# Optimization experiments

Measured on AMD Instinct MI355X. Metric: run time of the kernel, lower is better.

Reference implementation:

```python
import jax, jax.numpy as jnp
import numpy as np

NUM_LEVELS = 2
RADIUS = 3


def setup_inputs() -> dict:
    key = jax.random.key(0)
    k1, k2, k3 = jax.random.split(key, 3)
    x = jax.random.normal(k1, (4, 320, 9, 32, 32), dtype=jnp.float32)
    w_fc0 = jax.random.normal(k2, (160, 320), dtype=jnp.float32) * 0.05
    w_fc1 = jax.random.normal(k3, (160, 320), dtype=jnp.float32) * 0.05
    return {"x": x, "w_fc0": w_fc0, "w_fc1": w_fc1}


def _bilinear_zeros(img, xs, ys):
    # img: (M, H, W); xs, ys: (M, K) pixel coords.
    # Matches F.grid_sample(mode='bilinear', padding_mode='zeros', align_corners=True):
    # align_corners normalization round-trips to the raw pixel coords, and
    # out-of-bounds corners contribute zero.
    M, H, W = img.shape
    x0f = jnp.floor(xs)
    y0f = jnp.floor(ys)
    wx = xs - x0f
    wy = ys - y0f
    x0 = x0f.astype(jnp.int32)
    y0 = y0f.astype(jnp.int32)
    x1 = x0 + 1
    y1 = y0 + 1
    n = jnp.arange(M)[:, None]

    def corner(yi, xi):
        valid = (xi >= 0) & (xi < W) & (yi >= 0) & (yi < H)
        v = img[n, jnp.clip(yi, 0, H - 1), jnp.clip(xi, 0, W - 1)]
        return v * valid.astype(img.dtype)

    v00 = corner(y0, x0)
    v01 = corner(y0, x1)
    v10 = corner(y1, x0)
    v11 = corner(y1, x1)
    return (v00 * (1 - wx) * (1 - wy) + v01 * wx * (1 - wy)
            + v10 * (1 - wx) * wy + v11 * wx * wy)


def reference(x, w_fc0, w_fc1):
    b, c, T, h, w = x.shape
    xt = jnp.transpose(x, (0, 2, 1, 3, 4))  # (b, T, c, h, w)
    # 1x1 convs (no bias) on consecutive-frame pairs
    f0 = jnp.einsum('btchw,oc->bothw', xt[:, :-1], w_fc0)
    f1 = jnp.einsum('btchw,oc->bothw', xt[:, 1:], w_fc1)
    t = T - 1
    c2 = w_fc0.shape[0]
    f0 = f0.reshape(b * t, c2, h * w)
    f1 = f1.reshape(b * t, c2, h * w)
    # all-pairs correlation volume, normalized by channel count
    corr = jnp.einsum('nci,ncj->nij', f0, f1) / c2  # (bt, hw, hw)
    corr = corr.reshape(b * t * h * w, h, w)

    # pyramid via 2x2 avg pooling
    pyramid = [corr]
    for _ in range(NUM_LEVELS - 1):
        M, H, W = pyramid[-1].shape
        pyramid.append(pyramid[-1].reshape(M, H // 2, 2, W // 2, 2).mean(axis=(2, 4)))

    # per-pixel centroids (x, y), tiled over the bt batch axis
    ys, xs = jnp.meshgrid(jnp.arange(h), jnp.arange(w), indexing='ij')
    cx = jnp.tile(xs.reshape(-1).astype(jnp.float32), b * t)  # (bt*h*w,)
    cy = jnp.tile(ys.reshape(-1).astype(jnp.float32), b * t)

    # delta[i, j] = (d[i], d[j]); delta[...,0] -> x offset, delta[...,1] -> y offset
    r = RADIUS
    d = jnp.linspace(-r, r, 2 * r + 1)
    dx = jnp.repeat(d, 2 * r + 1)  # varies along first window dim
    dy = jnp.tile(d, 2 * r + 1)    # varies along second window dim

    outs = []
    for i, ci in enumerate(pyramid):
        xs_s = cx[:, None] / (2 ** i) + dx[None, :]  # (M, K)
        ys_s = cy[:, None] / (2 ** i) + dy[None, :]
        v = _bilinear_zeros(ci, xs_s, ys_s)          # (M, (2r+1)^2)
        outs.append(v.reshape(b * t, h, w, -1))
    out = jnp.concatenate(outs, axis=3)              # (bt, h, w, L*(2r+1)^2)
    out = out.reshape(b, t, h, w, -1)
    return jnp.transpose(out, (0, 4, 1, 2, 3)).astype(jnp.float32)
```

## Files before the change

### kernel.cpp

```cpp
#include <hip/hip_runtime.h>
#include <hip/hip_bf16.h>

typedef __attribute__((ext_vector_type(8))) short short8;
typedef __attribute__((ext_vector_type(4))) float f32x4;

static constexpr int HW = 1024;
static constexpr int C2 = 160;
static constexpr int FS = 168;
static constexpr int KSTEPS = 10;
static constexpr size_t PL = 32ull * 1024 * 160;
static constexpr size_t PPL = 32ull * 256 * 160;
static constexpr int AIMG = 6656;

__device__ inline short bfh(float v) {
  __hip_bfloat16 h = __float2bfloat16(v);
  return *reinterpret_cast<short*>(&h);
}
__device__ inline float bff(short s) {
  union { unsigned u; float f; } c;
  c.u = ((unsigned)(unsigned short)s) << 16;
  return c.f;
}

typedef const __attribute__((address_space(1))) void* gas_t;
typedef __attribute__((address_space(3))) void* las_t;
__device__ inline void gload_lds16(const void* g, void* l) {
  __builtin_amdgcn_global_load_lds((gas_t)g, (las_t)l, 16, 0, 0);
}

__global__ __launch_bounds__(256)
void wprep2_kernel(const float* __restrict__ w0, const float* __restrict__ w1,
                   short* __restrict__ wp) {
  const int id = blockIdx.x * 256 + threadIdx.x;
  if (id >= KSTEPS * 4 * AIMG) return;
  const int img = id / AIMG, r = id % AIMG;
  const int ks = img >> 2, qp = img & 3;
  short outv = 0;
  if (r < 6400) {
    const int hl = r / 3200;
    const int g2 = r % 3200;
    const int gr = g2 / 40, kk = g2 % 40;
    const int mat = gr >= 40;
    const int o = qp * 40 + gr - mat * 40;
    if (kk < 32) {
      const float v = (mat ? w1 : w0)[o * 320 + ks * 32 + kk];
      const short hb = bfh(v);
      outv = hl ? bfh(v - bff(hb)) : hb;
    }
  }
  wp[id] = outv;
}

__global__ __launch_bounds__(256)
void conv_fused(const float* __restrict__ x, const short* __restrict__ wprep2,
                short* __restrict__ f0bh, short* __restrict__ f0bl,
                short* __restrict__ f1bh, short* __restrict__ f1bl) {
  __shared__ __align__(16) char lds[50176];
  float* xF = reinterpret_cast<float*>(lds);
  short* aL = reinterpret_cast<short*>(lds + 36864);
  short* tL = reinterpret_cast<short*>(lds);

  const int pxt = blockIdx.x;
  const int qp = blockIdx.y;
  const int bb = blockIdx.z;
  const int tid = threadIdx.x;
  const int lane = tid & 63;
  const int wave = __builtin_amdgcn_readfirstlane(tid >> 6);
  const int lr = lane & 15, kg = lane >> 4;
  const int pxh = wave & 1;
  const int fpar = wave >> 1;

  const int l8 = lane >> 3;
  const int l7 = lane & 7;
  const int px = pxh * 16 + lr;
  const int pxs = px ^ (kg << 3);

  f32x4 acc[5][5];
#pragma unroll
  for (int mt = 0; mt < 5; ++mt)
#pragma unroll
    for (int fi = 0; fi < 5; ++fi)
#pragma unroll
      for (int r = 0; r < 4; ++r) acc[mt][fi][r] = 0.f;

  const float* xg = x + ((size_t)(bb * 320) * 9) * 1024 + (size_t)pxt * 32;

  for (int ks = 0; ks < KSTEPS; ++ks) {
    if (ks) __syncthreads();
    {
      const short* src = wprep2 + (size_t)(ks * 4 + qp) * AIMG;
#pragma unroll
      for (int jj = 0; jj < 4; ++jj) {
        const int j = wave * 4 + jj;
        if (j < 13) gload_lds16(src + j * 512 + lane * 8, aL + j * 512);
      }
    }
#pragma unroll
    for (int jj = 0; jj < 9; ++jj) {
      const int gi = wave * 9 + jj;
      const int f = gi >> 2, oct = gi & 3;
      const int c = ks * 32 + oct * 8 + l8;
      const float* src =
          xg + ((size_t)c * 9 + f) * 1024 + ((l7 ^ (oct << 1)) << 2);
      gload_lds16(src, xF + gi * 256);
    }
    __syncthreads();

    short8 Ah[5], Al[5];
#pragma unroll
    for (int mt = 0; mt < 5; ++mt) {
      Ah[mt] = *reinterpret_cast<const short8*>(&aL[(mt * 16 + lr) * 40 + kg * 8]);
      Al[mt] = *reinterpret_cast<const short8*>(&aL[3200 + (mt * 16 + lr) * 40 + kg * 8]);
    }
#pragma unroll
    for (int fi = 0; fi < 5; ++fi) {
      const int f = 2 * fi + fpar;
      if (f < 9) {
        const float* bp = xF + f * 1024 + kg * 256 + pxs;
        float xv[8];
#pragma unroll
        for (int j = 0; j < 8; ++j) xv[j] = bp[j * 32];
        short8 Bh, Bl;
#pragma unroll
        for (int j = 0; j < 8; ++j) {
          const short h = bfh(xv[j]);
          Bh[j] = h;
          Bl[j] = bfh(xv[j] - bff(h));
        }
#pragma unroll
        for (int mt = 0; mt < 5; ++mt) {
          acc[mt][fi] = __builtin_amdgcn_mfma_f32_16x16x32_bf16(Ah[mt], Bh, acc[mt][fi], 0, 0, 0);
          acc[mt][fi] = __builtin_amdgcn_mfma_f32_16x16x32_bf16(Ah[mt], Bl, acc[mt][fi], 0, 0, 0);
          acc[mt][fi] = __builtin_amdgcn_mfma_f32_16x16x32_bf16(Al[mt], Bh, acc[mt][fi], 0, 0, 0);
        }
      }
    }
  }

#pragma unroll
  for (int m = 0; m < 2; ++m) {
    __syncthreads();
#pragma unroll
    for (int mt = 0; mt < 5; ++mt)
#pragma unroll
      for (int fi = 0; fi < 5; ++fi) {
        const int f = 2 * fi + fpar;
        const int tt = f - m;
        if (f < 9 && (unsigned)tt < 8u) {
#pragma unroll
          for (int rr = 0; rr < 4; ++rr) {
            const int gr = mt * 16 + kg * 4 + rr;
            if ((gr >= 40) == (m == 1)) {
              const int rowl = gr - m * 40;
              const int ql = rowl / 20, r20 = rowl % 20;
              const int c = 8 * r20 + tt;
              const int row = ql * 32 + pxh * 16 + lr;
              const float v = acc[mt][fi][rr];
              const short h = bfh(v);
              const short l = bfh(v - bff(h));
              tL[row * FS + c] = h;
              tL[10752 + row * FS + c] = l;
            }
          }
        }
      }
    __syncthreads();
#pragma unroll
    for (int i = 0; i < 10; ++i) {
      const int idx = tid + i * 256;
      const int plane = idx / 1280, rem = idx % 1280;
      const int row = rem / 20, c16 = rem % 20;
      const int ql = row >> 5, pxl = row & 31;
      const int n = bb * 8 + qp * 2 + ql;
      short* dst = (m == 0) ? (plane ? f0bl : f0bh) : (plane ? f1bl : f1bh);
      *reinterpret_cast<uint4*>(dst + ((size_t)n * 1024 + pxt * 32 + pxl) * 160 + c16 * 8) =
          *reinterpret_cast<const uint4*>(&tL[plane * 10752 + row * FS + c16 * 8]);
    }
  }
}

__global__ __launch_bounds__(256)
void pool_b(const short* __restrict__ f1bh, const short* __restrict__ f1bl,
            short* __restrict__ g1pbh, short* __restrict__ g1pbl) {
  const int id = blockIdx.x * 256 + threadIdx.x;
  if (id >= 32 * 256 * 20) return;
  const int c16 = id % 20;
  const int PX = (id / 20) & 255;
  const int n = id / (20 * 256);
  const int Y = PX >> 4, X = PX & 15;
  const int r0 = Y * 64 + X * 2;
  const size_t base = ((size_t)n * 1024 + r0) * 160 + c16 * 8;
  const short8 h00 = *reinterpret_cast<const short8*>(f1bh + base);
  const short8 h01 = *reinterpret_cast<const short8*>(f1bh + base + 160);
  const short8 h10 = *reinterpret_cast<const short8*>(f1bh + base + 32 * 160);
  const short8 h11 = *reinterpret_cast<const short8*>(f1bh + base + 33 * 160);
  const short8 l00 = *reinterpret_cast<const short8*>(f1bl + base);
  const short8 l01 = *reinterpret_cast<const short8*>(f1bl + base + 160);
  const short8 l10 = *reinterpret_cast<const short8*>(f1bl + base + 32 * 160);
  const short8 l11 = *reinterpret_cast<const short8*>(f1bl + base + 33 * 160);
  short8 ho, lo;
#pragma unroll
  for (int j = 0; j < 8; ++j) {
    const float v = 0.25f * ((bff(h00[j]) + bff(l00[j])) + (bff(h01[j]) + bff(l01[j])) +
                             (bff(h10[j]) + bff(l10[j])) + (bff(h11[j]) + bff(l11[j])));
    const short h = bfh(v);
    ho[j] = h;
    lo[j] = bfh(v - bff(h));
  }
  const size_t ob = ((size_t)n * 256 + PX) * 160 + c16 * 8;
  *reinterpret_cast<short8*>(g1pbh + ob) = ho;
  *reinterpret_cast<short8*>(g1pbl + ob) = lo;
}

__global__ __launch_bounds__(256)
void corr_kernel(const short* __restrict__ f0bh, const short* __restrict__ f0bl,
                 const short* __restrict__ f1bh, const short* __restrict__ f1bl,
                 const short* __restrict__ g1pbh, const short* __restrict__ g1pbl,
                 float* __restrict__ out) {
  __shared__ __align__(16) short f0L[2][32 * FS];
  __shared__ __align__(16) short f1L[2][32 * FS];
  __shared__ float S0[32 * 33];
  __shared__ float S1[2][32 * 17];
  const int flat = blockIdx.x;
  const int xcd = flat & 7;
  const int rr_ = flat >> 3;
  const int y = rr_ & 31;
  const int n = (xcd << 2) | (rr_ >> 5);
  const int bb = n >> 3, q = n & 7;
  const int tid = threadIdx.x;
  const int lane = tid & 63;
  const int wave = __builtin_amdgcn_readfirstlane(tid >> 6);
  const int lr = lane & 15, kg = lane >> 4;
  const int xx = tid & 31;
  const int hi = tid >> 5;
  const float inv = 1.f / 160.f;
  const size_t obase = (size_t)(bb * 784 + q) * 1024 + (size_t)y * 32;

#pragma unroll
  for (int i = 0; i < 5; ++i) {
    const int idx = tid + i * 256;
    const int plane = idx / 640, rem = idx % 640;
    const int px = rem / 20, c16 = rem % 20;
    const short* src = (plane ? f0bl : f0bh) + ((size_t)n * 1024 + y * 32 + px) * 160 + c16 * 8;
    *reinterpret_cast<uint4*>(&f0L[plane][px * FS + c16 * 8]) =
        *reinterpret_cast<const uint4*>(src);
  }
  __syncthreads();

  const int mi0 = wave >> 1, ni0 = wave & 1;
  short8 a0h[5], a0l[5];
#pragma unroll
  for (int ks = 0; ks < 5; ++ks) {
    a0h[ks] = *reinterpret_cast<const short8*>(&f0L[0][(mi0 * 16 + lr) * FS + ks * 32 + kg * 8]);
    a0l[ks] = *reinterpret_cast<const short8*>(&f0L[1][(mi0 * 16 + lr) * FS + ks * 32 + kg * 8]);
  }

  for (int dyi = 0; dyi < 7; ++dyi) {
    const int yy = y + dyi - 3;
    const bool inr = (unsigned)yy < 32u;
    __syncthreads();
    if (inr) {
#pragma unroll
      for (int i = 0; i < 5; ++i) {
        const int idx = tid + i * 256;
        const int plane = idx / 640, rem = idx % 640;
        const int px = rem / 20, c16 = rem % 20;
        const short* src = (plane ? f1bl : f1bh) + ((size_t)n * 1024 + yy * 32 + px) * 160 + c16 * 8;
        *reinterpret_cast<uint4*>(&f1L[plane][px * FS + c16 * 8]) =
            *reinterpret_cast<const uint4*>(src);
      }
    }
    __syncthreads();
    if (inr) {
      f32x4 aA = {0.f, 0.f, 0.f, 0.f}, aB = aA, aC = aA;
#pragma unroll
      for (int ks = 0; ks < 5; ++ks) {
        const short8 bh = *reinterpret_cast<const short8*>(&f1L[0][(ni0 * 16 + lr) * FS + ks * 32 + kg * 8]);
        const short8 bl = *reinterpret_cast<const short8*>(&f1L[1][(ni0 * 16 + lr) * FS + ks * 32 + kg * 8]);
        aA = __builtin_amdgcn_mfma_f32_16x16x32_bf16(a0h[ks], bh, aA, 0, 0, 0);
        aB = __builtin_amdgcn_mfma_f32_16x16x32_bf16(a0h[ks], bl, aB, 0, 0, 0);
        aC = __builtin_amdgcn_mfma_f32_16x16x32_bf16(a0l[ks], bh, aC, 0, 0, 0);
      }
#pragma unroll
      for (int r = 0; r < 4; ++r)
        S0[(mi0 * 16 + kg * 4 + r) * 33 + ni0 * 16 + lr] = (aA[r] + aB[r]) + aC[r];
    }
    __syncthreads();
    if (hi < 7) {
      const int x2 = xx + hi - 3;
      const float val = (inr && (unsigned)x2 < 32u) ? S0[xx * 33 + x2] * inv : 0.f;
      out[obase + (size_t)(hi * 7 + dyi) * 8192 + xx] = val;
    }
  }

  short8 a1h[5], a1l[5];
  if (wave < 2) {
#pragma unroll
    for (int ks = 0; ks < 5; ++ks) {
      a1h[ks] = *reinterpret_cast<const short8*>(&f0L[0][(wave * 16 + lr) * FS + ks * 32 + kg * 8]);
      a1l[ks] = *reinterpret_cast<const short8*>(&f0L[1][(wave * 16 + lr) * FS + ks * 32 + kg * 8]);
    }
  }
  const int Y0 = (y >> 1) - 3;
  const float wy = (y & 1) ? 0.5f : 0.f;
  for (int v = 0; v < 8; ++v) {
    const int Y = Y0 + v;
    const bool inr = (unsigned)Y < 16u;
    __syncthreads();
    if (inr) {
#pragma unroll
      for (int i = 0; i < 3; ++i) {
        const int idx = tid + i * 256;
        if (idx < 640) {
          const int plane = idx / 320, rem = idx % 320;
          const int px = rem / 20, c16 = rem % 20;
          const short* src = (plane ? g1pbl : g1pbh) + ((size_t)n * 256 + Y * 16 + px) * 160 + c16 * 8;
          *reinterpret_cast<uint4*>(&f1L[plane][px * FS + c16 * 8]) =
              *reinterpret_cast<const uint4*>(src);
        }
      }
    }
    __syncthreads();
    if (wave < 2) {
      f32x4 aA = {0.f, 0.f, 0.f, 0.f}, aB = aA, aC = aA;
      if (inr) {
#pragma unroll
        for (int ks = 0; ks < 5; ++ks) {
          const short8 bh = *reinterpret_cast<const short8*>(&f1L[0][lr * FS + ks * 32 + kg * 8]);
          const short8 bl = *reinterpret_cast<const short8*>(&f1L[1][lr * FS + ks * 32 + kg * 8]);
          aA = __builtin_amdgcn_mfma_f32_16x16x32_bf16(a1h[ks], bh, aA, 0, 0, 0);
          aB = __builtin_amdgcn_mfma_f32_16x16x32_bf16(a1h[ks], bl, aB, 0, 0, 0);
          aC = __builtin_amdgcn_mfma_f32_16x16x32_bf16(a1l[ks], bh, aC, 0, 0, 0);
        }
      }
#pragma unroll
      for (int r = 0; r < 4; ++r)
        S1[v & 1][(wave * 16 + kg * 4 + r) * 17 + lr] = (aA[r] + aB[r]) + aC[r];
    }
    __syncthreads();
    if (v >= 1 && hi < 7) {
      const int dyi = v - 1;
      const int Xl = (xx >> 1) - 3 + hi;
      const int Xr = Xl + 1;
      const float* t0 = S1[(v - 1) & 1];
      const float* t1 = S1[v & 1];
      const float a00 = ((unsigned)Xl < 16u) ? t0[xx * 17 + Xl] : 0.f;
      const float a01 = ((unsigned)Xr < 16u) ? t0[xx * 17 + Xr] : 0.f;
      const float a10 = ((unsigned)Xl < 16u) ? t1[xx * 17 + Xl] : 0.f;
      const float a11 = ((unsigned)Xr < 16u) ? t1[xx * 17 + Xr] : 0.f;
      const float wx = (xx & 1) ? 0.5f : 0.f;
      const float val = ((1.f - wx) * ((1.f - wy) * a00 + wy * a10) +
                         wx * ((1.f - wy) * a01 + wy * a11)) * inv;
      out[obase + (size_t)(49 + hi * 7 + dyi) * 8192 + xx] = val;
    }
  }
}

extern "C" void kernel_launch(void* const* d_in, const int* in_sizes, int n_in,
                              void* d_out, int out_size, void* d_ws,
                              size_t ws_size, hipStream_t stream) {
  const float* x = (const float*)d_in[0];
  const float* w0 = (const float*)d_in[1];
  const float* w1 = (const float*)d_in[2];
  short* f0bh = (short*)d_ws;
  short* f0bl = f0bh + PL;
  short* f1bh = f0bl + PL;
  short* f1bl = f1bh + PL;
  short* g1pbh = f1bl + PL;
  short* g1pbl = g1pbh + PPL;
  short* wprep2 = g1pbh;
  float* out = (float*)d_out;

  wprep2_kernel<<<1040, 256, 0, stream>>>(w0, w1, wprep2);
  conv_fused<<<dim3(32, 4, 4), 256, 0, stream>>>(x, wprep2, f0bh, f0bl, f1bh, f1bl);
  pool_b<<<640, 256, 0, stream>>>(f1bh, f1bl, g1pbh, g1pbl);
  corr_kernel<<<1024, 256, 0, stream>>>(f0bh, f0bl, f1bh, f1bl, g1pbh, g1pbl, out);
}
```

Before: 82.97 us.

## Halve conv pixel tile to double grid, use direct-to-LDS loads in corr

The conv kernel now processes 16 pixels per block instead of 32. It launches twice as many blocks and uses less LDS per block, and each wave owns frames rather than a pixel half and frame parity. The correlation kernel swaps per-thread uint4 copies into padded LDS rows for contiguous global-to-LDS direct loads into unpadded 160-wide rows. This trades padding that avoided bank conflicts for simpler, wider loads. The intent is more occupancy and parallelism in conv and cheaper staging in corr, at the risk of LDS bank conflicts on the unpadded reads and more redundant weight loads per block.

```diff
diff --git a/kernel.cpp b/kernel.cpp
--- a/kernel.cpp
+++ b/kernel.cpp
@@ -7,6 +7,7 @@
 static constexpr int HW = 1024;
 static constexpr int C2 = 160;
 static constexpr int FS = 168;
+static constexpr int FSC = 160;
 static constexpr int KSTEPS = 10;
 static constexpr size_t PL = 32ull * 1024 * 160;
 static constexpr size_t PPL = 32ull * 256 * 160;
@@ -55,9 +56,9 @@
 void conv_fused(const float* __restrict__ x, const short* __restrict__ wprep2,
                 short* __restrict__ f0bh, short* __restrict__ f0bl,
                 short* __restrict__ f1bh, short* __restrict__ f1bl) {
-  __shared__ __align__(16) char lds[50176];
+  __shared__ __align__(16) char lds[31744];
   float* xF = reinterpret_cast<float*>(lds);
-  short* aL = reinterpret_cast<short*>(lds + 36864);
+  short* aL = reinterpret_cast<short*>(lds + 18432);
   short* tL = reinterpret_cast<short*>(lds);
 
   const int pxt = blockIdx.x;
@@ -67,23 +68,16 @@
   const int lane = tid & 63;
   const int wave = __builtin_amdgcn_readfirstlane(tid >> 6);
   const int lr = lane & 15, kg = lane >> 4;
-  const int pxh = wave & 1;
-  const int fpar = wave >> 1;
-
-  const int l8 = lane >> 3;
-  const int l7 = lane & 7;
-  const int px = pxh * 16 + lr;
-  const int pxs = px ^ (kg << 3);
-
-  f32x4 acc[5][5];
+
+  f32x4 acc[5][3];
 #pragma unroll
   for (int mt = 0; mt < 5; ++mt)
 #pragma unroll
-    for (int fi = 0; fi < 5; ++fi)
+    for (int fi = 0; fi < 3; ++fi)
 #pragma unroll
       for (int r = 0; r < 4; ++r) acc[mt][fi][r] = 0.f;
 
-  const float* xg = x + ((size_t)(bb * 320) * 9) * 1024 + (size_t)pxt * 32;
+  const float* xg = x + ((size_t)(bb * 320) * 9) * 1024 + (size_t)pxt * 16;
 
   for (int ks = 0; ks < KSTEPS; ++ks) {
     if (ks) __syncthreads();
@@ -96,13 +90,14 @@
       }
     }
 #pragma unroll
-    for (int jj = 0; jj < 9; ++jj) {
-      const int gi = wave * 9 + jj;
-      const int f = gi >> 2, oct = gi & 3;
-      const int c = ks * 32 + oct * 8 + l8;
-      const float* src =
-          xg + ((size_t)c * 9 + f) * 1024 + ((l7 ^ (oct << 1)) << 2);
-      gload_lds16(src, xF + gi * 256);
+    for (int jj = 0; jj < 5; ++jj) {
+      const int gi = wave * 5 + jj;
+      if (gi < 18) {
+        const int f = gi >> 1, half = gi & 1;
+        const int c = ks * 32 + half * 16 + (lane >> 2);
+        const float* src = xg + ((size_t)c * 9 + f) * 1024 + (lane & 3) * 4;
+        gload_lds16(src, xF + gi * 256);
+      }
     }
     __syncthreads();
 
@@ -113,13 +108,13 @@
       Al[mt] = *reinterpret_cast<const short8*>(&aL[3200 + (mt * 16 + lr) * 40 + kg * 8]);
     }
 #pragma unroll
-    for (int fi = 0; fi < 5; ++fi) {
-      const int f = 2 * fi + fpar;
+    for (int fi = 0; fi < 3; ++fi) {
+      const int f = wave + fi * 4;
       if (f < 9) {
-        const float* bp = xF + f * 1024 + kg * 256 + pxs;
+        const float* bp = xF + f * 512 + kg * 128 + lr;
         float xv[8];
 #pragma unroll
-        for (int j = 0; j < 8; ++j) xv[j] = bp[j * 32];
+        for (int j = 0; j < 8; ++j) xv[j] = bp[j * 16];
         short8 Bh, Bl;
 #pragma unroll
         for (int j = 0; j < 8; ++j) {
@@ -143,8 +138,8 @@
 #pragma unroll
     for (int mt = 0; mt < 5; ++mt)
 #pragma unroll
-      for (int fi = 0; fi < 5; ++fi) {
-        const int f = 2 * fi + fpar;
+      for (int fi = 0; fi < 3; ++fi) {
+        const int f = wave + fi * 4;
         const int tt = f - m;
         if (f < 9 && (unsigned)tt < 8u) {
 #pragma unroll
@@ -154,27 +149,26 @@
               const int rowl = gr - m * 40;
               const int ql = rowl / 20, r20 = rowl % 20;
               const int c = 8 * r20 + tt;
-              const int row = ql * 32 + pxh * 16 + lr;
+              const int row = ql * 16 + lr;
               const float v = acc[mt][fi][rr];
               const short h = bfh(v);
-              const short l = bfh(v - bff(h));
               tL[row * FS + c] = h;
-              tL[10752 + row * FS + c] = l;
+              tL[5376 + row * FS + c] = bfh(v - bff(h));
             }
           }
         }
       }
     __syncthreads();
 #pragma unroll
-    for (int i = 0; i < 10; ++i) {
+    for (int i = 0; i < 5; ++i) {
       const int idx = tid + i * 256;
-      const int plane = idx / 1280, rem = idx % 1280;
+      const int plane = idx / 640, rem = idx % 640;
       const int row = rem / 20, c16 = rem % 20;
-      const int ql = row >> 5, pxl = row & 31;
+      const int ql = row >> 4, pxl = row & 15;
       const int n = bb * 8 + qp * 2 + ql;
       short* dst = (m == 0) ? (plane ? f0bl : f0bh) : (plane ? f1bl : f1bh);
-      *reinterpret_cast<uint4*>(dst + ((size_t)n * 1024 + pxt * 32 + pxl) * 160 + c16 * 8) =
-          *reinterpret_cast<const uint4*>(&tL[plane * 10752 + row * FS + c16 * 8]);
+      *reinterpret_cast<uint4*>(dst + ((size_t)n * 1024 + pxt * 16 + pxl) * 160 + c16 * 8) =
+          *reinterpret_cast<const uint4*>(&tL[plane * 5376 + row * FS + c16 * 8]);
     }
   }
 }
@@ -217,8 +211,8 @@
                  const short* __restrict__ f1bh, const short* __restrict__ f1bl,
                  const short* __restrict__ g1pbh, const short* __restrict__ g1pbl,
                  float* __restrict__ out) {
-  __shared__ __align__(16) short f0L[2][32 * FS];
-  __shared__ __align__(16) short f1L[2][32 * FS];
+  __shared__ __align__(16) short f0L[2][32 * FSC];
+  __shared__ __align__(16) short f1L[2][32 * FSC];
   __shared__ float S0[32 * 33];
   __shared__ float S1[2][32 * 17];
   const int flat = blockIdx.x;
@@ -236,14 +230,15 @@
   const float inv = 1.f / 160.f;
   const size_t obase = (size_t)(bb * 784 + q) * 1024 + (size_t)y * 32;
 
-#pragma unroll
-  for (int i = 0; i < 5; ++i) {
-    const int idx = tid + i * 256;
-    const int plane = idx / 640, rem = idx % 640;
-    const int px = rem / 20, c16 = rem % 20;
-    const short* src = (plane ? f0bl : f0bh) + ((size_t)n * 1024 + y * 32 + px) * 160 + c16 * 8;
-    *reinterpret_cast<uint4*>(&f0L[plane][px * FS + c16 * 8]) =
-        *reinterpret_cast<const uint4*>(src);
+  {
+    const short* s0 = f0bh + ((size_t)n * 1024 + y * 32) * 160;
+    const short* s1 = f0bl + ((size_t)n * 1024 + y * 32) * 160;
+#pragma unroll
+    for (int jj = 0; jj < 5; ++jj) {
+      const int j = wave * 5 + jj;
+      const int pl = j / 10, off = (j % 10) * 512;
+      gload_lds16((pl ? s1 : s0) + off + lane * 8, &f0L[pl][off]);
+    }
   }
   __syncthreads();
 
@@ -251,8 +246,8 @@
   short8 a0h[5], a0l[5];
 #pragma unroll
   for (int ks = 0; ks < 5; ++ks) {
-    a0h[ks] = *reinterpret_cast<const short8*>(&f0L[0][(mi0 * 16 + lr) * FS + ks * 32 + kg * 8]);
-    a0l[ks] = *reinterpret_cast<const short8*>(&f0L[1][(mi0 * 16 + lr) * FS + ks * 32 + kg * 8]);
+    a0h[ks] = *reinterpret_cast<const short8*>(&f0L[0][(mi0 * 16 + lr) * FSC + ks * 32 + kg * 8]);
+    a0l[ks] = *reinterpret_cast<const short8*>(&f0L[1][(mi0 * 16 + lr) * FSC + ks * 32 + kg * 8]);
   }
 
   for (int dyi = 0; dyi < 7; ++dyi) {
@@ -260,14 +255,13 @@
     const bool inr = (unsigned)yy < 32u;
     __syncthreads();
     if (inr) {
-#pragma unroll
-      for (int i = 0; i < 5; ++i) {
-        const int idx = tid + i * 256;
-        const int plane = idx / 640, rem = idx % 640;
-        const int px = rem / 20, c16 = rem % 20;
-        const short* src = (plane ? f1bl : f1bh) + ((size_t)n * 1024 + yy * 32 + px) * 160 + c16 * 8;
-        *reinterpret_cast<uint4*>(&f1L[plane][px * FS + c16 * 8]) =
-            *reinterpret_cast<const uint4*>(src);
+      const short* s0 = f1bh + ((size_t)n * 1024 + yy * 32) * 160;
+      const short* s1 = f1bl + ((size_t)n * 1024 + yy * 32) * 160;
+#pragma unroll
+      for (int jj = 0; jj < 5; ++jj) {
+        const int j = wave * 5 + jj;
+        const int pl = j / 10, off = (j % 10) * 512;
+        gload_lds16((pl ? s1 : s0) + off + lane * 8, &f1L[pl][off]);
       }
     }
     __syncthreads();
@@ -275,8 +269,8 @@
       f32x4 aA = {0.f, 0.f, 0.f, 0.f}, aB = aA, aC = aA;
 #pragma unroll
       for (int ks = 0; ks < 5; ++ks) {
-        const short8 bh = *reinterpret_cast<const short8*>(&f1L[0][(ni0 * 16 + lr) * FS + ks * 32 + kg * 8]);
-        const short8 bl = *reinterpret_cast<const short8*>(&f1L[1][(ni0 * 16 + lr) * FS + ks * 32 + kg * 8]);
+        const short8 bh = *reinterpret_cast<const short8*>(&f1L[0][(ni0 * 16 + lr) * FSC + ks * 32 + kg * 8]);
+        const short8 bl = *reinterpret_cast<const short8*>(&f1L[1][(ni0 * 16 + lr) * FSC + ks * 32 + kg * 8]);
         aA = __builtin_amdgcn_mfma_f32_16x16x32_bf16(a0h[ks], bh, aA, 0, 0, 0);
         aB = __builtin_amdgcn_mfma_f32_16x16x32_bf16(a0h[ks], bl, aB, 0, 0, 0);
         aC = __builtin_amdgcn_mfma_f32_16x16x32_bf16(a0l[ks], bh, aC, 0, 0, 0);
@@ -297,8 +291,8 @@
   if (wave < 2) {
 #pragma unroll
     for (int ks = 0; ks < 5; ++ks) {
-      a1h[ks] = *reinterpret_cast<const short8*>(&f0L[0][(wave * 16 + lr) * FS + ks * 32 + kg * 8]);
-      a1l[ks] = *reinterpret_cast<const short8*>(&f0L[1][(wave * 16 + lr) * FS + ks * 32 + kg * 8]);
+      a1h[ks] = *reinterpret_cast<const short8*>(&f0L[0][(wave * 16 + lr) * FSC + ks * 32 + kg * 8]);
+      a1l[ks] = *reinterpret_cast<const short8*>(&f0L[1][(wave * 16 + lr) * FSC + ks * 32 + kg * 8]);
     }
   }
   const int Y0 = (y >> 1) - 3;
@@ -308,15 +302,14 @@
     const bool inr = (unsigned)Y < 16u;
     __syncthreads();
     if (inr) {
-#pragma unroll
-      for (int i = 0; i < 3; ++i) {
-        const int idx = tid + i * 256;
-        if (idx < 640) {
-          const int plane = idx / 320, rem = idx % 320;
-          const int px = rem / 20, c16 = rem % 20;
-          const short* src = (plane ? g1pbl : g1pbh) + ((size_t)n * 256 + Y * 16 + px) * 160 + c16 * 8;
-          *reinterpret_cast<uint4*>(&f1L[plane][px * FS + c16 * 8]) =
-              *reinterpret_cast<const uint4*>(src);
+      const short* s0 = g1pbh + ((size_t)n * 256 + Y * 16) * 160;
+      const short* s1 = g1pbl + ((size_t)n * 256 + Y * 16) * 160;
+#pragma unroll
+      for (int jj = 0; jj < 3; ++jj) {
+        const int j = wave * 3 + jj;
+        if (j < 10) {
+          const int pl = j / 5, off = (j % 5) * 512;
+          gload_lds16((pl ? s1 : s0) + off + lane * 8, &f1L[pl][off]);
         }
       }
     }
@@ -326,8 +319,8 @@
       if (inr) {
 #pragma unroll
         for (int ks = 0; ks < 5; ++ks) {
-          const short8 bh = *reinterpret_cast<const short8*>(&f1L[0][lr * FS + ks * 32 + kg * 8]);
-          const short8 bl = *reinterpret_cast<const short8*>(&f1L[1][lr * FS + ks * 32 + kg * 8]);
+          const short8 bh = *reinterpret_cast<const short8*>(&f1L[0][lr * FSC + ks * 32 + kg * 8]);
+          const short8 bl = *reinterpret_cast<const short8*>(&f1L[1][lr * FSC + ks * 32 + kg * 8]);
           aA = __builtin_amdgcn_mfma_f32_16x16x32_bf16(a1h[ks], bh, aA, 0, 0, 0);
           aB = __builtin_amdgcn_mfma_f32_16x16x32_bf16(a1h[ks], bl, aB, 0, 0, 0);
           aC = __builtin_amdgcn_mfma_f32_16x16x32_bf16(a1l[ks], bh, aC, 0, 0, 0);
@@ -372,7 +365,7 @@
   float* out = (float*)d_out;
 
   wprep2_kernel<<<1040, 256, 0, stream>>>(w0, w1, wprep2);
-  conv_fused<<<dim3(32, 4, 4), 256, 0, stream>>>(x, wprep2, f0bh, f0bl, f1bh, f1bl);
+  conv_fused<<<dim3(64, 4, 4), 256, 0, stream>>>(x, wprep2, f0bh, f0bl, f1bh, f1bl);
   pool_b<<<640, 256, 0, stream>>>(f1bh, f1bl, g1pbh, g1pbl);
   corr_kernel<<<1024, 256, 0, stream>>>(f0bh, f0bl, f1bh, f1bl, g1pbh, g1pbl, out);
 }
```

Result: slower. 84.90 us (+2.3%).
